# Optimization experiments

Hardware: AMD Instinct MI355X
Metric: run time of the kernel (lower is better)

The kernel has to match this reference:

```python
import jax, jax.numpy as jnp
import numpy as np

COMMITMENT_COST = 0.25
EPSILON = 1e-05


def setup_inputs() -> dict:
    key = jax.random.key(0)
    k1, k2, k3 = jax.random.split(key, 3)
    inputs = jax.random.normal(k1, (32, 256, 32, 32), dtype=jnp.float32)
    embedding = jax.random.normal(k2, (256, 1024), dtype=jnp.float32)
    cluster_size = jax.random.uniform(k3, (1024,), dtype=jnp.float32)
    return {"inputs": inputs, "embedding": embedding, "cluster_size": cluster_size}


def reference(inputs, embedding, cluster_size):
    B = inputs.shape[0]
    D, K = embedding.shape  # (embedding_dim, num_embeddings)

    # Faithful to source: reshape (B,C,H,W) -> (-1, D) WITHOUT permuting.
    flat_input = inputs.reshape(-1, D)  # (N, D), N = B*H*W (since C == D)

    distances = (
        jnp.sum(flat_input ** 2, axis=1, keepdims=True)
        + jnp.sum(embedding ** 2, axis=0, keepdims=True)
        - 2.0 * flat_input @ embedding
    )  # (N, K)
    encoding_indices = jnp.argmin(distances, axis=1)  # (N,)

    # Gather codes: embedding[:, idx].T -> (N, D), reshape back to input shape
    quantized = jnp.take(embedding, encoding_indices, axis=1).T.reshape(inputs.shape)

    e_latent_loss = jnp.mean((jax.lax.stop_gradient(quantized) - inputs) ** 2)
    q_latent_loss = jnp.mean((quantized - jax.lax.stop_gradient(inputs)) ** 2)
    commitment_loss = COMMITMENT_COST * q_latent_loss
    vq_loss = e_latent_loss + commitment_loss

    # Straight-through estimator
    quantized_ste = inputs + jax.lax.stop_gradient(quantized - inputs)

    avg_probs = cluster_size / (jnp.sum(cluster_size) + EPSILON)
    perplexity = jnp.exp(-jnp.sum(avg_probs * jnp.log(avg_probs + EPSILON)))
    used_codes = jnp.sum((cluster_size > EPSILON).astype(jnp.float32))
    code_usage_rate = used_codes / K

    return (quantized_ste, vq_loss, perplexity, code_usage_rate,
            encoding_indices.reshape(B, -1))
```

## Files before the change

kernel.cpp:

```cpp
#include <hip/hip_runtime.h>


constexpr int DIM = 256;
constexpr int NK  = 1024;
constexpr int RR  = 16;

#define GLL16(GSRC, LDST)                                                      \
  __builtin_amdgcn_global_load_lds(                                            \
      (const __attribute__((address_space(1))) void*)(GSRC),                   \
      (__attribute__((address_space(3))) void*)(LDST), 16, 0, 0)

__global__ __launch_bounds__(256) void enorm_kernel(
    const float* __restrict__ emb, float* __restrict__ enorm) {
  int k = blockIdx.x * 256 + threadIdx.x;
  float s = 0.f;
  for (int d = 0; d < DIM; ++d) {
    float e = emb[(size_t)d * NK + k];
    s = fmaf(e, e, s);
  }
  enorm[k] = 0.5f * s;
}

#define STAGE(G, P)                                                            \
  { const float* _s = emb + ((size_t)(4 * (G)) << 10) + k0;                    \
    GLL16(_s,          &es[(P)][0][k0]);                                       \
    GLL16(_s + NK,     &es[(P)][1][k0]);                                       \
    GLL16(_s + 2 * NK, &es[(P)][2][k0]);                                       \
    GLL16(_s + 3 * NK, &es[(P)][3][k0]); }

#define XLOAD(XA, G)                                                           \
  _Pragma("unroll")                                                            \
  for (int r = 0; r < RR; ++r)                                                 \
    XA[r] = *(const float4*)&xg[r * DIM + 4 * (G)];

#define COMPUTE4(PAR, XA)                                                      \
  { const float4 e0 = *(const float4*)&es[(PAR)][0][k0];                       \
    const float4 e1 = *(const float4*)&es[(PAR)][1][k0];                       \
    const float4 e2 = *(const float4*)&es[(PAR)][2][k0];                       \
    const float4 e3 = *(const float4*)&es[(PAR)][3][k0];                       \
    _Pragma("unroll")                                                          \
    for (int r = 0; r < RR; ++r) {                                             \
      const float4 xv = XA[r];                                                 \
      acc[r][0] = fmaf(xv.x, e0.x, fmaf(xv.y, e1.x, fmaf(xv.z, e2.x, fmaf(xv.w, e3.x, acc[r][0])))); \
      acc[r][1] = fmaf(xv.x, e0.y, fmaf(xv.y, e1.y, fmaf(xv.z, e2.y, fmaf(xv.w, e3.y, acc[r][1])))); \
      acc[r][2] = fmaf(xv.x, e0.z, fmaf(xv.y, e1.z, fmaf(xv.z, e2.z, fmaf(xv.w, e3.z, acc[r][2])))); \
      acc[r][3] = fmaf(xv.x, e0.w, fmaf(xv.y, e1.w, fmaf(xv.z, e2.w, fmaf(xv.w, e3.w, acc[r][3])))); \
    } }

#define SB __builtin_amdgcn_sched_barrier(0);

__global__ __launch_bounds__(256, 2) void argmin_kernel(
    const float* __restrict__ x, const float* __restrict__ emb,
    const float* __restrict__ enorm, int* __restrict__ idx_out,
    float* __restrict__ idx_out_f) {
  __shared__ float es[2][4][NK];
  __shared__ float red_v[4][RR];
  __shared__ int   red_i[4][RR];

  const int tid  = threadIdx.x;
  const int lane = tid & 63;
  const int wv   = tid >> 6;
  const int k0   = tid * 4;
  const float* xg = x + (size_t)blockIdx.x * (RR * DIM);

  STAGE(0, 0)
  STAGE(1, 1)
  asm volatile("s_waitcnt vmcnt(4)" ::: "memory");
  SB

  float4 xA[RR], xB[RR];
  XLOAD(xA, 0)

  float acc[RR][4];
  #pragma unroll
  for (int r = 0; r < RR; ++r)
    #pragma unroll
    for (int j = 0; j < 4; ++j) acc[r][j] = 0.f;

  #pragma unroll 1
  for (int gg = 0; gg < 32; ++gg) {
    const int g0 = 2 * gg;
    const int g1 = g0 + 1;

    asm volatile("s_waitcnt vmcnt(4)" ::: "memory");
    SB
    XLOAD(xB, g1)
    COMPUTE4(0, xA)
    SB
    if (gg <= 30) STAGE(g0 + 2, 0)

    if (gg < 31) {
      asm volatile("s_waitcnt vmcnt(4)" ::: "memory");
    } else {
      asm volatile("s_waitcnt vmcnt(0)" ::: "memory");
    }
    SB
    if (gg <= 30) XLOAD(xA, g1 + 1)
    COMPUTE4(1, xB)
    SB
    if (gg <= 30) STAGE(g1 + 2, 1)
  }

  const float4 en = *(const float4*)(enorm + k0);

  for (int r = 0; r < RR; ++r) {
    float bv = en.x - acc[r][0];
    int   bi = k0;
    { float v = en.y - acc[r][1]; if (v < bv) { bv = v; bi = k0 + 1; } }
    { float v = en.z - acc[r][2]; if (v < bv) { bv = v; bi = k0 + 2; } }
    { float v = en.w - acc[r][3]; if (v < bv) { bv = v; bi = k0 + 3; } }
    for (int off = 32; off > 0; off >>= 1) {
      float ov = __shfl_xor(bv, off);
      int   oi = __shfl_xor(bi, off);
      if (ov < bv || (ov == bv && oi < bi)) { bv = ov; bi = oi; }
    }
    if (lane == 0) { red_v[wv][r] = bv; red_i[wv][r] = bi; }
  }
  __syncthreads();

  if (tid < RR) {
    float bv = red_v[0][tid];
    int   bi = red_i[0][tid];
    #pragma unroll
    for (int w = 1; w < 4; ++w) {
      float v = red_v[w][tid]; int i2 = red_i[w][tid];
      if (v < bv || (v == bv && i2 < bi)) { bv = v; bi = i2; }
    }
    const int n = blockIdx.x * RR + tid;
    idx_out[n]   = bi;
    idx_out_f[n] = (float)bi;
  }
}

__global__ __launch_bounds__(256) void gather_loss_kernel(
    const float* __restrict__ x, const float* __restrict__ emb,
    const int* __restrict__ idx, float* __restrict__ out_q,
    float* __restrict__ partial) {
  const int tid = threadIdx.x;
  const size_t base = (size_t)blockIdx.x * 2048;
  float local = 0.f;
  #pragma unroll
  for (int h = 0; h < 2; ++h) {
    const size_t g = base + (size_t)h * 1024 + (size_t)tid * 4;
    const int n = (int)(g >> 8);
    const int d = (int)(g & 255);
    const int k = idx[n];
    const float* ep = emb + (size_t)d * NK + k;
    float4 q;
    q.x = ep[0]; q.y = ep[NK]; q.z = ep[2 * NK]; q.w = ep[3 * NK];
    const float4 xv = *(const float4*)(x + g);
    *(float4*)(out_q + g) = q;
    const float dx = q.x - xv.x, dy = q.y - xv.y, dz = q.z - xv.z, dw = q.w - xv.w;
    local = fmaf(dx, dx, local);
    local = fmaf(dy, dy, local);
    local = fmaf(dz, dz, local);
    local = fmaf(dw, dw, local);
  }
  for (int off = 32; off > 0; off >>= 1) local += __shfl_down(local, off);
  __shared__ float wsum[4];
  if ((tid & 63) == 0) wsum[tid >> 6] = local;
  __syncthreads();
  if (tid == 0) partial[blockIdx.x] = (wsum[0] + wsum[1]) + (wsum[2] + wsum[3]);
}

__global__ __launch_bounds__(1024) void finalize_kernel(
    const float* __restrict__ partial, int np,
    const float* __restrict__ cs, float* __restrict__ out_s,
    float inv_count) {
  __shared__ float sd[1024];
  const int tid = threadIdx.x;

  float s = 0.f;
  for (int i = tid; i < np; i += 1024) s += partial[i];
  sd[tid] = s; __syncthreads();
  for (int st = 512; st > 0; st >>= 1) {
    if (tid < st) sd[tid] += sd[tid + st];
    __syncthreads();
  }
  const float total_sq = sd[0];
  __syncthreads();

  const float c = cs[tid];
  sd[tid] = c; __syncthreads();
  for (int st = 512; st > 0; st >>= 1) {
    if (tid < st) sd[tid] += sd[tid + st];
    __syncthreads();
  }
  const float S = sd[0];
  __syncthreads();

  const float p = c / (S + 1e-5f);
  sd[tid] = p * logf(p + 1e-5f);
  __syncthreads();
  for (int st = 512; st > 0; st >>= 1) {
    if (tid < st) sd[tid] += sd[tid + st];
    __syncthreads();
  }
  const float T = sd[0];
  __syncthreads();

  sd[tid] = (c > 1e-5f) ? 1.f : 0.f;
  __syncthreads();
  for (int st = 512; st > 0; st >>= 1) {
    if (tid < st) sd[tid] += sd[tid + st];
    __syncthreads();
  }
  const float U = sd[0];

  if (tid == 0) {
    out_s[0] = 1.25f * total_sq * inv_count;
    out_s[1] = expf(-T);
    out_s[2] = U * (1.f / 1024.f);
  }
}

extern "C" void kernel_launch(void* const* d_in, const int* in_sizes, int n_in,
                              void* d_out, int out_size, void* d_ws, size_t ws_size,
                              hipStream_t stream) {
  const float* x   = (const float*)d_in[0];
  const float* emb = (const float*)d_in[1];
  const float* cs  = (const float*)d_in[2];
  float* out = (float*)d_out;

  const int N = in_sizes[0] / DIM;
  const size_t ND = (size_t)N * DIM;

  float* enorm   = (float*)d_ws;
  int*   idxw    = (int*)((char*)d_ws + NK * sizeof(float));
  float* partial = (float*)((char*)d_ws + NK * sizeof(float) + (size_t)N * sizeof(int));

  const int nGather = (int)(ND / 2048);

  enorm_kernel<<<NK / 256, 256, 0, stream>>>(emb, enorm);
  argmin_kernel<<<N / RR, 256, 0, stream>>>(x, emb, enorm, idxw, out + ND + 3);
  gather_loss_kernel<<<nGather, 256, 0, stream>>>(x, emb, idxw, out, partial);
  finalize_kernel<<<1, 1024, 0, stream>>>(partial, nGather, cs, out + ND,
                                          1.0f / (float)ND);
}
```

Measured before the change: 348.9 us.

## Halve rows per argmin block, raise occupancy, hoist LDS codebook reads

```diff
diff --git a/kernel.cpp b/kernel.cpp
--- a/kernel.cpp
+++ b/kernel.cpp
@@ -3,12 +3,14 @@
 
 constexpr int DIM = 256;
 constexpr int NK  = 1024;
-constexpr int RR  = 16;
+constexpr int RR  = 8;
 
 #define GLL16(GSRC, LDST)                                                      \
   __builtin_amdgcn_global_load_lds(                                            \
       (const __attribute__((address_space(1))) void*)(GSRC),                   \
       (__attribute__((address_space(3))) void*)(LDST), 16, 0, 0)
+
+#define SB __builtin_amdgcn_sched_barrier(0);
 
 __global__ __launch_bounds__(256) void enorm_kernel(
     const float* __restrict__ emb, float* __restrict__ enorm) {
@@ -33,23 +35,17 @@
   for (int r = 0; r < RR; ++r)                                                 \
     XA[r] = *(const float4*)&xg[r * DIM + 4 * (G)];
 
-#define COMPUTE4(PAR, XA)                                                      \
-  { const float4 e0 = *(const float4*)&es[(PAR)][0][k0];                       \
-    const float4 e1 = *(const float4*)&es[(PAR)][1][k0];                       \
-    const float4 e2 = *(const float4*)&es[(PAR)][2][k0];                       \
-    const float4 e3 = *(const float4*)&es[(PAR)][3][k0];                       \
-    _Pragma("unroll")                                                          \
-    for (int r = 0; r < RR; ++r) {                                             \
-      const float4 xv = XA[r];                                                 \
-      acc[r][0] = fmaf(xv.x, e0.x, fmaf(xv.y, e1.x, fmaf(xv.z, e2.x, fmaf(xv.w, e3.x, acc[r][0])))); \
-      acc[r][1] = fmaf(xv.x, e0.y, fmaf(xv.y, e1.y, fmaf(xv.z, e2.y, fmaf(xv.w, e3.y, acc[r][1])))); \
-      acc[r][2] = fmaf(xv.x, e0.z, fmaf(xv.y, e1.z, fmaf(xv.z, e2.z, fmaf(xv.w, e3.z, acc[r][2])))); \
-      acc[r][3] = fmaf(xv.x, e0.w, fmaf(xv.y, e1.w, fmaf(xv.z, e2.w, fmaf(xv.w, e3.w, acc[r][3])))); \
-    } }
-
-#define SB __builtin_amdgcn_sched_barrier(0);
-
-__global__ __launch_bounds__(256, 2) void argmin_kernel(
+#define FMA8(XA)                                                               \
+  _Pragma("unroll")                                                            \
+  for (int r = 0; r < RR; ++r) {                                               \
+    const float4 xv = XA[r];                                                   \
+    acc[r][0] = fmaf(xv.x, e0.x, fmaf(xv.y, e1.x, fmaf(xv.z, e2.x, fmaf(xv.w, e3.x, acc[r][0])))); \
+    acc[r][1] = fmaf(xv.x, e0.y, fmaf(xv.y, e1.y, fmaf(xv.z, e2.y, fmaf(xv.w, e3.y, acc[r][1])))); \
+    acc[r][2] = fmaf(xv.x, e0.z, fmaf(xv.y, e1.z, fmaf(xv.z, e2.z, fmaf(xv.w, e3.z, acc[r][2])))); \
+    acc[r][3] = fmaf(xv.x, e0.w, fmaf(xv.y, e1.w, fmaf(xv.z, e2.w, fmaf(xv.w, e3.w, acc[r][3])))); \
+  }
+
+__global__ __launch_bounds__(256, 4) void argmin_kernel(
     const float* __restrict__ x, const float* __restrict__ emb,
     const float* __restrict__ enorm, int* __restrict__ idx_out,
     float* __restrict__ idx_out_f) {
@@ -65,8 +61,6 @@
 
   STAGE(0, 0)
   STAGE(1, 1)
-  asm volatile("s_waitcnt vmcnt(4)" ::: "memory");
-  SB
 
   float4 xA[RR], xB[RR];
   XLOAD(xA, 0)
@@ -82,23 +76,36 @@
     const int g0 = 2 * gg;
     const int g1 = g0 + 1;
 
-    asm volatile("s_waitcnt vmcnt(4)" ::: "memory");
-    SB
-    XLOAD(xB, g1)
-    COMPUTE4(0, xA)
-    SB
-    if (gg <= 30) STAGE(g0 + 2, 0)
-
-    if (gg < 31) {
+    {
       asm volatile("s_waitcnt vmcnt(4)" ::: "memory");
-    } else {
-      asm volatile("s_waitcnt vmcnt(0)" ::: "memory");
-    }
-    SB
-    if (gg <= 30) XLOAD(xA, g1 + 1)
-    COMPUTE4(1, xB)
-    SB
-    if (gg <= 30) STAGE(g1 + 2, 1)
+      SB
+      const float4 e0 = *(const float4*)&es[0][0][k0];
+      const float4 e1 = *(const float4*)&es[0][1][k0];
+      const float4 e2 = *(const float4*)&es[0][2][k0];
+      const float4 e3 = *(const float4*)&es[0][3][k0];
+      asm volatile("s_waitcnt lgkmcnt(0)" ::: "memory");
+      SB
+      XLOAD(xB, g1)
+      SB
+      FMA8(xA)
+      SB
+      if (gg <= 30) STAGE(g0 + 2, 0)
+    }
+    {
+      if (gg < 31) { asm volatile("s_waitcnt vmcnt(4)" ::: "memory"); }
+      else         { asm volatile("s_waitcnt vmcnt(0)" ::: "memory"); }
+      SB
+      const float4 e0 = *(const float4*)&es[1][0][k0];
+      const float4 e1 = *(const float4*)&es[1][1][k0];
+      const float4 e2 = *(const float4*)&es[1][2][k0];
+      const float4 e3 = *(const float4*)&es[1][3][k0];
+      asm volatile("s_waitcnt lgkmcnt(0)" ::: "memory");
+      SB
+      if (gg <= 30) { XLOAD(xA, g0 + 2) SB }
+      FMA8(xB)
+      SB
+      if (gg <= 30) STAGE(g1 + 2, 1)
+    }
   }
 
   const float4 en = *(const float4*)(enorm + k0);
```

New measurement: 290.6 us. 16.7% less time.
